# Performance work log

Hardware: AMD Instinct MI355X
Metric: run time of the kernel (lower is better)

The kernel has to match this reference:

```python
import jax, jax.numpy as jnp
import numpy as np
from jax import lax

B, C, H, W = 4, 256, 64, 64
C8 = C // 8  # 32


def setup_inputs() -> dict:
    key = jax.random.key(0)
    ks = jax.random.split(key, 8)
    x = jax.random.normal(ks[0], (B, C, H, W), jnp.float32)
    # 1x1 conv weights stored as [out_ch, in_ch]
    wb = jax.random.normal(ks[1], (C8, 2 * C), jnp.float32) * 0.02
    bb = jax.random.normal(ks[2], (C8,), jnp.float32) * 0.02
    wc = jax.random.normal(ks[3], (C8, 2 * C), jnp.float32) * 0.02
    bc = jax.random.normal(ks[4], (C8,), jnp.float32) * 0.02
    wd = jax.random.normal(ks[5], (C, 2 * C), jnp.float32) * 0.02
    bd = jax.random.normal(ks[6], (C,), jnp.float32) * 0.02
    alpha = jnp.float32(0.5)  # nn.Parameter(zeros(1)) at init; nonzero for a meaningful test
    return {"x": x, "wb": wb, "bb": bb, "wc": wc, "bc": bc, "wd": wd, "bd": bd, "alpha": alpha}


def reference(x, wb, bb, wc, bc, wd, bd, alpha):
    b, c, h, w = x.shape
    n = h * w
    pad = [(0, 0), (0, 0), (1, 1), (1, 1)]
    # F.avg_pool2d(k=3, s=1, p=1) with count_include_pad=True -> window-sum / 9
    x_avg = lax.reduce_window(x, 0.0, lax.add, (1, 1, 3, 3), (1, 1, 1, 1), pad) / 9.0
    x_max = lax.reduce_window(x, -jnp.inf, lax.max, (1, 1, 3, 3), (1, 1, 1, 1), pad)
    cat = jnp.concatenate([x_avg, x_max], axis=1)  # [B, 2C, H, W]
    catf = cat.reshape(b, 2 * c, n)                # [B, 2C, N]
    # 1x1 convs == per-pixel linear projections
    feat_b = jnp.einsum('oc,bcn->bon', wb, catf) + bb[None, :, None]  # [B, C8, N]
    feat_c = jnp.einsum('oc,bcn->bon', wc, catf) + bc[None, :, None]  # [B, C8, N]
    feat_d = jnp.einsum('oc,bcn->bon', wd, catf) + bd[None, :, None]  # [B, C,  N]
    # attention_s = softmax(feat_b^T @ feat_c) over last dim -> [B, N, N]
    attn = jax.nn.softmax(jnp.einsum('bon,bom->bnm', feat_b, feat_c), axis=-1)
    # feat_e = feat_d @ attn^T -> [B, C, N]
    feat_e = jnp.einsum('bcn,bmn->bcm', feat_d, attn).reshape(b, c, h, w)
    return alpha * feat_e + (1.0 - alpha) * x
```

## Files before the change

### kernel.cpp

```cpp
#include <hip/hip_runtime.h>
#include <hip/hip_bf16.h>

typedef __hip_bfloat16 bf16;
typedef __attribute__((ext_vector_type(8))) short s8v;
typedef __attribute__((ext_vector_type(4))) float f4v;

__device__ __forceinline__ ushort f2u(float f) {
    bf16 h = __float2bfloat16(f);
    return *(ushort*)&h;
}


__global__ __launch_bounds__(256) void pool_kernel(
    const float* __restrict__ x, ushort* __restrict__ cat,
    const float* __restrict__ wb, const float* __restrict__ wc,
    const float* __restrict__ wd, ushort* __restrict__ Wf) {
    int bid = blockIdx.x;
    int tid = threadIdx.x;
    if (bid >= 1024) {
        int f = (bid - 1024) * 4 + (tid >> 6);
        int l = tid & 63;
        int ot = f % 20, kc = f / 20;
        int o = ot * 16 + (l & 15);
        int k0 = kc * 32 + (l >> 4) * 8;
        const float* wr = (o < 32) ? wb + (size_t)o * 512
                        : (o < 64) ? wc + (size_t)(o - 32) * 512
                                   : wd + (size_t)(o - 64) * 512;
        float4 f0 = *(const float4*)(wr + k0);
        float4 f1 = *(const float4*)(wr + k0 + 4);
        ushort tmp[8] = {f2u(f0.x), f2u(f0.y), f2u(f0.z), f2u(f0.w),
                         f2u(f1.x), f2u(f1.y), f2u(f1.z), f2u(f1.w)};
        *(uint4*)(Wf + kc * 10240 + ot * 512 + l * 8) = *(uint4*)tmp;
        return;
    }
    __shared__ float Xs[3][64][66];
    int b = bid >> 8, h = (bid >> 2) & 63, cg = bid & 3;
    bool hasU = (h > 0), hasD = (h < 63);
    #pragma unroll
    for (int pp = 0; pp < 12; ++pp) {
        int linear = pp * 256 + tid;
        int w4 = linear & 15;
        int cs = (linear >> 4) & 63;
        int dh = linear >> 10;
        int hh = h + dh - 1;
        float4 f = {0.f, 0.f, 0.f, 0.f};
        if ((unsigned)hh < 64u)
            f = *(const float4*)(x + ((size_t)(b * 256 + cg * 64 + cs)) * 4096
                                 + hh * 64 + w4 * 4);
        Xs[dh][w4 * 4 + 0][cs] = f.x;
        Xs[dh][w4 * 4 + 1][cs] = f.y;
        Xs[dh][w4 * 4 + 2][cs] = f.z;
        Xs[dh][w4 * 4 + 3][cs] = f.w;
    }
    __syncthreads();
    int cs = tid & 63, ws = tid >> 6;
    float vs[18], vm[18];
    #pragma unroll
    for (int j = 0; j < 18; ++j) {
        int w = ws * 16 - 1 + j;
        if ((unsigned)w < 64u) {
            float u = Xs[0][w][cs], m = Xs[1][w][cs], d = Xs[2][w][cs];
            vs[j] = u + m + d;
            float mx = m;
            if (hasU) mx = fmaxf(mx, u);
            if (hasD) mx = fmaxf(mx, d);
            vm[j] = mx;
        } else { vs[j] = 0.f; vm[j] = -3.4e38f; }
    }
    size_t nb = ((size_t)b * 4096 + h * 64 + ws * 16) * 512 + cg * 64 + cs;
    #pragma unroll
    for (int i = 0; i < 16; ++i) {
        float sum = vs[i] + vs[i + 1] + vs[i + 2];
        float mx  = fmaxf(fmaxf(vm[i], vm[i + 1]), vm[i + 2]);
        cat[nb + (size_t)i * 512]       = f2u(sum * (1.f / 9.f));
        cat[nb + (size_t)i * 512 + 256] = f2u(mx);
    }
}

__global__ __launch_bounds__(256, 2) void proj_kernel(
    const ushort* __restrict__ cat, const ushort* __restrict__ Wf,
    const float* __restrict__ bb, const float* __restrict__ bc,
    const float* __restrict__ bd,
    ushort* __restrict__ Qb, ushort* __restrict__ Kb, ushort* __restrict__ Vf) {
    __shared__ __align__(16) ushort As[32][72];
    __shared__ __align__(16) ushort Vls[256][40];
    int tid = threadIdx.x;
    int l = tid & 63, w = tid >> 6;
    int lm = l & 15, q = l >> 4;
    int n0 = blockIdx.x * 32;
    f4v acc[2][5];
    #pragma unroll
    for (int mt = 0; mt < 2; ++mt)
        #pragma unroll
        for (int ot = 0; ot < 5; ++ot)
            #pragma unroll
            for (int i = 0; i < 4; ++i) acc[mt][ot][i] = 0.f;

    const ushort* wfb = Wf + (w * 5) * 512 + l * 8;
    int sr = tid >> 3, sko = (tid & 7) * 8;
    const ushort* srow = cat + (size_t)(n0 + sr) * 512 + sko;

    for (int kc = 0; kc < 8; ++kc) {
        *(uint4*)&As[sr][sko] = *(const uint4*)(srow + kc * 64);
        __syncthreads();
        #pragma unroll
        for (int ks = 0; ks < 2; ++ks) {
            int kci = kc * 2 + ks;
            s8v bf[5];
            #pragma unroll
            for (int ot = 0; ot < 5; ++ot)
                bf[ot] = *(const s8v*)(wfb + kci * 10240 + ot * 512);
            s8v a0 = *(const s8v*)&As[lm][ks * 32 + q * 8];
            s8v a1 = *(const s8v*)&As[16 + lm][ks * 32 + q * 8];
            #pragma unroll
            for (int ot = 0; ot < 5; ++ot) {
                acc[0][ot] = __builtin_amdgcn_mfma_f32_16x16x32_bf16(a0, bf[ot], acc[0][ot], 0, 0, 0);
                acc[1][ot] = __builtin_amdgcn_mfma_f32_16x16x32_bf16(a1, bf[ot], acc[1][ot], 0, 0, 0);
            }
        }
        __syncthreads();
    }
    #pragma unroll
    for (int ot = 0; ot < 5; ++ot) {
        int o = w * 80 + ot * 16 + lm;
        if (o < 32) {
            float bias = bb[o];
            #pragma unroll
            for (int mt = 0; mt < 2; ++mt)
                #pragma unroll
                for (int r = 0; r < 4; ++r)
                    Qb[(size_t)(n0 + mt * 16 + q * 4 + r) * 32 + o]
                        = f2u(acc[mt][ot][r] + bias);
        } else if (o < 64) {
            float bias = bc[o - 32];
            #pragma unroll
            for (int mt = 0; mt < 2; ++mt)
                #pragma unroll
                for (int r = 0; r < 4; ++r)
                    Kb[(size_t)(n0 + mt * 16 + q * 4 + r) * 32 + (o - 32)]
                        = f2u(acc[mt][ot][r] + bias);
        } else {
            int c = o - 64;
            float bias = bd[c];
            #pragma unroll
            for (int mt = 0; mt < 2; ++mt) {
                ushort tmp[4];
                #pragma unroll
                for (int r = 0; r < 4; ++r) tmp[r] = f2u(acc[mt][ot][r] + bias);
                *(uint2*)&Vls[c][mt * 16 + q * 4] = *(uint2*)tmp;
            }
        }
    }
    __syncthreads();
    {
        int bidx = n0 >> 12;
        size_t fb = ((size_t)bidx << 20) + (size_t)((n0 & 4095) >> 5) * 8192 + l * 8;
        #pragma unroll
        for (int i = 0; i < 4; ++i) {
            int cb = w * 4 + i;
            *(uint4*)(Vf + fb + cb * 512) = *(const uint4*)&Vls[cb * 16 + lm][q * 8];
        }
    }
}

__global__ __launch_bounds__(512, 2) void attn_kernel(
    const ushort* __restrict__ Qb, const ushort* __restrict__ Kb,
    const ushort* __restrict__ Vf, const float* __restrict__ x,
    const float* __restrict__ alphap, float* __restrict__ out) {
    __shared__ __align__(16) ushort Ps[2][64][72];
    __shared__ float Obuf[4][64][17];
    __shared__ float Lpart[4][64];
    __shared__ float Lrow[64];
    int tid = threadIdx.x;
    int l = tid & 63, w = tid >> 6;
    int lm = l & 15, q = l >> 4;
    int nsw = w & 3, kh = w >> 2;
    int bid = blockIdx.x;
    int xcd = bid & 7;
    int b = xcd & 3;
    int midx = (bid >> 3) + ((xcd >> 2) << 5);
    int m0 = midx << 6;
    size_t bN = (size_t)b << 12;

    s8v Qf[2];
    {
        const ushort* qb = Qb + (bN + m0 + kh * 32) * 32;
        Qf[0] = *(const s8v*)(qb + (size_t)(lm) * 32 + q * 8);
        Qf[1] = *(const s8v*)(qb + (size_t)(16 + lm) * 32 + q * 8);
    }
    const ushort* kbp = Kb + (bN + nsw * 16 + lm) * 32 + q * 8;
    const ushort* vfp = Vf + ((size_t)b << 20) + kh * 8192 + (nsw * 4) * 512 + l * 8;

    f4v acc[4][4];
    #pragma unroll
    for (int mt = 0; mt < 4; ++mt)
        #pragma unroll
        for (int ct = 0; ct < 4; ++ct)
            #pragma unroll
            for (int i = 0; i < 4; ++i) acc[mt][ct][i] = 0.f;
    float La0 = 0.f, La1 = 0.f;

    s8v kf0 = *(const s8v*)kbp;
    s8v kf1 = *(const s8v*)(kbp + 2048);
    s8v vfA[4], vfB[4];
    #pragma unroll
    for (int ct = 0; ct < 4; ++ct) vfA[ct] = *(const s8v*)(vfp + ct * 512);
    {
        f4v S0 = {0.f, 0.f, 0.f, 0.f}, S1 = {0.f, 0.f, 0.f, 0.f};
        S0 = __builtin_amdgcn_mfma_f32_16x16x32_bf16(kf0, Qf[0], S0, 0, 0, 0);
        S1 = __builtin_amdgcn_mfma_f32_16x16x32_bf16(kf0, Qf[1], S1, 0, 0, 0);
        ushort e0[4], e1[4];
        #pragma unroll
        for (int r = 0; r < 4; ++r) {
            float f0 = __expf(fminf(S0[r], 60.f));
            float f1 = __expf(fminf(S1[r], 60.f));
            La0 += f0; La1 += f1;
            e0[r] = f2u(f0); e1[r] = f2u(f1);
        }
        *(uint2*)&Ps[0][kh * 32 + lm][nsw * 16 + q * 4]      = *(uint2*)e0;
        *(uint2*)&Ps[0][kh * 32 + 16 + lm][nsw * 16 + q * 4] = *(uint2*)e1;
    }
    __syncthreads();

#define TILE_BODY(TT, KFS, KFP, VCUR, VNXT)                                       \
    {                                                                             \
        int p = (TT) & 1;                                                         \
        if ((TT) < 63) {                                                          \
            f4v S0 = {0.f, 0.f, 0.f, 0.f}, S1 = {0.f, 0.f, 0.f, 0.f};             \
            S0 = __builtin_amdgcn_mfma_f32_16x16x32_bf16(KFS, Qf[0], S0, 0, 0, 0);\
            S1 = __builtin_amdgcn_mfma_f32_16x16x32_bf16(KFS, Qf[1], S1, 0, 0, 0);\
            ushort e0[4], e1[4];                                                  \
            _Pragma("unroll")                                                     \
            for (int r = 0; r < 4; ++r) {                                         \
                float f0 = __expf(fminf(S0[r], 60.f));                            \
                float f1 = __expf(fminf(S1[r], 60.f));                            \
                La0 += f0; La1 += f1;                                             \
                e0[r] = f2u(f0); e1[r] = f2u(f1);                                 \
            }                                                                     \
            *(uint2*)&Ps[1 - p][kh * 32 + lm][nsw * 16 + q * 4]      = *(uint2*)e0;\
            *(uint2*)&Ps[1 - p][kh * 32 + 16 + lm][nsw * 16 + q * 4] = *(uint2*)e1;\
        }                                                                         \
        if ((TT) < 62) KFP = *(const s8v*)(kbp + (size_t)((TT) + 2) * 2048);      \
        if ((TT) < 63) {                                                          \
            const ushort* vn = vfp + (size_t)((TT) + 1) * 16384;                  \
            _Pragma("unroll")                                                     \
            for (int ct = 0; ct < 4; ++ct)                                        \
                VNXT[ct] = *(const s8v*)(vn + ct * 512);                          \
        }                                                                         \
        s8v Af0 = *(const s8v*)&Ps[p][lm][kh * 32 + q * 8];                       \
        s8v Af1 = *(const s8v*)&Ps[p][16 + lm][kh * 32 + q * 8];                  \
        s8v Af2 = *(const s8v*)&Ps[p][32 + lm][kh * 32 + q * 8];                  \
        s8v Af3 = *(const s8v*)&Ps[p][48 + lm][kh * 32 + q * 8];                  \
        _Pragma("unroll")                                                         \
        for (int ct = 0; ct < 4; ++ct) {                                          \
            acc[0][ct] = __builtin_amdgcn_mfma_f32_16x16x32_bf16(Af0, VCUR[ct], acc[0][ct], 0, 0, 0); \
            acc[1][ct] = __builtin_amdgcn_mfma_f32_16x16x32_bf16(Af1, VCUR[ct], acc[1][ct], 0, 0, 0); \
            acc[2][ct] = __builtin_amdgcn_mfma_f32_16x16x32_bf16(Af2, VCUR[ct], acc[2][ct], 0, 0, 0); \
            acc[3][ct] = __builtin_amdgcn_mfma_f32_16x16x32_bf16(Af3, VCUR[ct], acc[3][ct], 0, 0, 0); \
        }                                                                         \
        __syncthreads();                                                          \
    }

    for (int t = 0; t < 64; t += 2) {
        TILE_BODY(t,     kf1, kf0, vfA, vfB);
        TILE_BODY(t + 1, kf0, kf1, vfB, vfA);
    }
#undef TILE_BODY

    La0 += __shfl_xor(La0, 16, 64); La0 += __shfl_xor(La0, 32, 64);
    La1 += __shfl_xor(La1, 16, 64); La1 += __shfl_xor(La1, 32, 64);
    if (q == 0) {
        Lpart[nsw][kh * 32 + lm]      = La0;
        Lpart[nsw][kh * 32 + 16 + lm] = La1;
    }
    __syncthreads();
    if (tid < 64)
        Lrow[tid] = Lpart[0][tid] + Lpart[1][tid] + Lpart[2][tid] + Lpart[3][tid];
    __syncthreads();
    #pragma unroll
    for (int ct = 0; ct < 4; ++ct) {
        if (kh == 1) {
            #pragma unroll
            for (int mt = 0; mt < 4; ++mt)
                #pragma unroll
                for (int r = 0; r < 4; ++r)
                    Obuf[nsw][mt * 16 + q * 4 + r][lm] = acc[mt][ct][r];
        }
        __syncthreads();
        if (kh == 0) {
            #pragma unroll
            for (int mt = 0; mt < 4; ++mt)
                #pragma unroll
                for (int r = 0; r < 4; ++r)
                    acc[mt][ct][r] += Obuf[nsw][mt * 16 + q * 4 + r][lm];
        }
        __syncthreads();
    }
    if (kh == 0) {
        float alpha = alphap[0];
        float ra = 1.f - alpha;
        #pragma unroll
        for (int mt = 0; mt < 4; ++mt) {
            float L0 = Lrow[mt * 16 + q * 4 + 0];
            float L1 = Lrow[mt * 16 + q * 4 + 1];
            float L2 = Lrow[mt * 16 + q * 4 + 2];
            float L3 = Lrow[mt * 16 + q * 4 + 3];
            #pragma unroll
            for (int ct = 0; ct < 4; ++ct) {
                int cc = nsw * 64 + ct * 16 + lm;
                size_t base = ((size_t)(b * 256 + cc)) * 4096 + m0 + mt * 16 + q * 4;
                float4 xv = *(const float4*)(x + base);
                float4 ov;
                ov.x = alpha * (acc[mt][ct][0] / L0) + ra * xv.x;
                ov.y = alpha * (acc[mt][ct][1] / L1) + ra * xv.y;
                ov.z = alpha * (acc[mt][ct][2] / L2) + ra * xv.z;
                ov.w = alpha * (acc[mt][ct][3] / L3) + ra * xv.w;
                *(float4*)(out + base) = ov;
            }
        }
    }
}

extern "C" void kernel_launch(void* const* d_in, const int* in_sizes, int n_in,
                              void* d_out, int out_size, void* d_ws, size_t ws_size,
                              hipStream_t stream) {
    const float* x  = (const float*)d_in[0];
    const float* wb = (const float*)d_in[1];
    const float* bb = (const float*)d_in[2];
    const float* wc = (const float*)d_in[3];
    const float* bc = (const float*)d_in[4];
    const float* wd = (const float*)d_in[5];
    const float* bd = (const float*)d_in[6];
    const float* al = (const float*)d_in[7];
    float* out = (float*)d_out;

    char* ws = (char*)d_ws;
    ushort* cat = (ushort*)ws;
    ushort* Qb  = (ushort*)(ws + 16777216);
    ushort* Kb  = (ushort*)(ws + 17825792);
    ushort* Vf  = (ushort*)(ws + 18874368);
    ushort* Wf  = (ushort*)(ws + 27262976);

    pool_kernel<<<dim3(1104), dim3(256), 0, stream>>>(x, cat, wb, wc, wd, Wf);
    proj_kernel<<<dim3(512), dim3(256), 0, stream>>>(cat, Wf, bb, bc, bd,
                                                     Qb, Kb, Vf);
    attn_kernel<<<dim3(256), dim3(512), 0, stream>>>(Qb, Kb, Vf, x, al, out);
}
```

Measured before the change: 164.6 us.

## Double attention block to 1024 threads, split S and channels across more waves

The attention kernel now runs 16 waves per block instead of 8. Each wave computes one 16x16 S tile instead of two and accumulates 32 output channels instead of 64, which halves per-wave MFMA work and register pressure. The exp/P-store for the next tile is moved after the PV MFMAs so it can overlap with them, and the final normalisation uses reciprocals instead of divisions. The cost is more block-wide synchronisation across twice as many waves, plus a larger Obuf in shared memory. The launch bound of (1024,4) may force a register cap that causes spills.

```diff
diff --git a/kernel.cpp b/kernel.cpp
--- a/kernel.cpp
+++ b/kernel.cpp
@@ -163,18 +163,19 @@
     }
 }
 
-__global__ __launch_bounds__(512, 2) void attn_kernel(
+__global__ __launch_bounds__(1024, 4) void attn_kernel(
     const ushort* __restrict__ Qb, const ushort* __restrict__ Kb,
     const ushort* __restrict__ Vf, const float* __restrict__ x,
     const float* __restrict__ alphap, float* __restrict__ out) {
     __shared__ __align__(16) ushort Ps[2][64][72];
-    __shared__ float Obuf[4][64][17];
+    __shared__ float Obuf[8][64][17];
     __shared__ float Lpart[4][64];
     __shared__ float Lrow[64];
     int tid = threadIdx.x;
     int l = tid & 63, w = tid >> 6;
     int lm = l & 15, q = l >> 4;
-    int nsw = w & 3, kh = w >> 2;
+    int nsw = w & 3, msw = w >> 2;
+    int cs = w & 7, kh = w >> 3;
     int bid = blockIdx.x;
     int xcd = bid & 7;
     int b = xcd & 3;
@@ -182,82 +183,69 @@
     int m0 = midx << 6;
     size_t bN = (size_t)b << 12;
 
-    s8v Qf[2];
-    {
-        const ushort* qb = Qb + (bN + m0 + kh * 32) * 32;
-        Qf[0] = *(const s8v*)(qb + (size_t)(lm) * 32 + q * 8);
-        Qf[1] = *(const s8v*)(qb + (size_t)(16 + lm) * 32 + q * 8);
-    }
+    s8v Qf = *(const s8v*)(Qb + (bN + m0 + msw * 16 + lm) * 32 + q * 8);
     const ushort* kbp = Kb + (bN + nsw * 16 + lm) * 32 + q * 8;
-    const ushort* vfp = Vf + ((size_t)b << 20) + kh * 8192 + (nsw * 4) * 512 + l * 8;
-
-    f4v acc[4][4];
+    const ushort* vfp = Vf + ((size_t)b << 20) + kh * 8192 + (2 * cs) * 512 + l * 8;
+
+    f4v acc[4][2];
     #pragma unroll
     for (int mt = 0; mt < 4; ++mt)
         #pragma unroll
-        for (int ct = 0; ct < 4; ++ct)
+        for (int ct = 0; ct < 2; ++ct)
             #pragma unroll
             for (int i = 0; i < 4; ++i) acc[mt][ct][i] = 0.f;
-    float La0 = 0.f, La1 = 0.f;
+    float La = 0.f;
 
     s8v kf0 = *(const s8v*)kbp;
     s8v kf1 = *(const s8v*)(kbp + 2048);
-    s8v vfA[4], vfB[4];
-    #pragma unroll
-    for (int ct = 0; ct < 4; ++ct) vfA[ct] = *(const s8v*)(vfp + ct * 512);
+    s8v vfA[2], vfB[2];
+    vfA[0] = *(const s8v*)(vfp);
+    vfA[1] = *(const s8v*)(vfp + 512);
     {
-        f4v S0 = {0.f, 0.f, 0.f, 0.f}, S1 = {0.f, 0.f, 0.f, 0.f};
-        S0 = __builtin_amdgcn_mfma_f32_16x16x32_bf16(kf0, Qf[0], S0, 0, 0, 0);
-        S1 = __builtin_amdgcn_mfma_f32_16x16x32_bf16(kf0, Qf[1], S1, 0, 0, 0);
-        ushort e0[4], e1[4];
+        f4v S = {0.f, 0.f, 0.f, 0.f};
+        S = __builtin_amdgcn_mfma_f32_16x16x32_bf16(kf0, Qf, S, 0, 0, 0);
+        ushort e0[4];
         #pragma unroll
         for (int r = 0; r < 4; ++r) {
-            float f0 = __expf(fminf(S0[r], 60.f));
-            float f1 = __expf(fminf(S1[r], 60.f));
-            La0 += f0; La1 += f1;
-            e0[r] = f2u(f0); e1[r] = f2u(f1);
-        }
-        *(uint2*)&Ps[0][kh * 32 + lm][nsw * 16 + q * 4]      = *(uint2*)e0;
-        *(uint2*)&Ps[0][kh * 32 + 16 + lm][nsw * 16 + q * 4] = *(uint2*)e1;
+            float f0 = __expf(fminf(S[r], 60.f));
+            La += f0; e0[r] = f2u(f0);
+        }
+        *(uint2*)&Ps[0][msw * 16 + lm][nsw * 16 + q * 4] = *(uint2*)e0;
     }
     __syncthreads();
 
 #define TILE_BODY(TT, KFS, KFP, VCUR, VNXT)                                       \
     {                                                                             \
         int p = (TT) & 1;                                                         \
-        if ((TT) < 63) {                                                          \
-            f4v S0 = {0.f, 0.f, 0.f, 0.f}, S1 = {0.f, 0.f, 0.f, 0.f};             \
-            S0 = __builtin_amdgcn_mfma_f32_16x16x32_bf16(KFS, Qf[0], S0, 0, 0, 0);\
-            S1 = __builtin_amdgcn_mfma_f32_16x16x32_bf16(KFS, Qf[1], S1, 0, 0, 0);\
-            ushort e0[4], e1[4];                                                  \
-            _Pragma("unroll")                                                     \
-            for (int r = 0; r < 4; ++r) {                                         \
-                float f0 = __expf(fminf(S0[r], 60.f));                            \
-                float f1 = __expf(fminf(S1[r], 60.f));                            \
-                La0 += f0; La1 += f1;                                             \
-                e0[r] = f2u(f0); e1[r] = f2u(f1);                                 \
-            }                                                                     \
-            *(uint2*)&Ps[1 - p][kh * 32 + lm][nsw * 16 + q * 4]      = *(uint2*)e0;\
-            *(uint2*)&Ps[1 - p][kh * 32 + 16 + lm][nsw * 16 + q * 4] = *(uint2*)e1;\
-        }                                                                         \
+        f4v S = {0.f, 0.f, 0.f, 0.f};                                             \
+        if ((TT) < 63)                                                            \
+            S = __builtin_amdgcn_mfma_f32_16x16x32_bf16(KFS, Qf, S, 0, 0, 0);     \
         if ((TT) < 62) KFP = *(const s8v*)(kbp + (size_t)((TT) + 2) * 2048);      \
         if ((TT) < 63) {                                                          \
             const ushort* vn = vfp + (size_t)((TT) + 1) * 16384;                  \
-            _Pragma("unroll")                                                     \
-            for (int ct = 0; ct < 4; ++ct)                                        \
-                VNXT[ct] = *(const s8v*)(vn + ct * 512);                          \
+            VNXT[0] = *(const s8v*)(vn);                                          \
+            VNXT[1] = *(const s8v*)(vn + 512);                                    \
         }                                                                         \
         s8v Af0 = *(const s8v*)&Ps[p][lm][kh * 32 + q * 8];                       \
         s8v Af1 = *(const s8v*)&Ps[p][16 + lm][kh * 32 + q * 8];                  \
         s8v Af2 = *(const s8v*)&Ps[p][32 + lm][kh * 32 + q * 8];                  \
         s8v Af3 = *(const s8v*)&Ps[p][48 + lm][kh * 32 + q * 8];                  \
         _Pragma("unroll")                                                         \
-        for (int ct = 0; ct < 4; ++ct) {                                          \
+        for (int ct = 0; ct < 2; ++ct) {                                          \
             acc[0][ct] = __builtin_amdgcn_mfma_f32_16x16x32_bf16(Af0, VCUR[ct], acc[0][ct], 0, 0, 0); \
             acc[1][ct] = __builtin_amdgcn_mfma_f32_16x16x32_bf16(Af1, VCUR[ct], acc[1][ct], 0, 0, 0); \
             acc[2][ct] = __builtin_amdgcn_mfma_f32_16x16x32_bf16(Af2, VCUR[ct], acc[2][ct], 0, 0, 0); \
             acc[3][ct] = __builtin_amdgcn_mfma_f32_16x16x32_bf16(Af3, VCUR[ct], acc[3][ct], 0, 0, 0); \
         }                                                                         \
+        if ((TT) < 63) {                                                          \
+            ushort e0[4];                                                         \
+            _Pragma("unroll")                                                     \
+            for (int r = 0; r < 4; ++r) {                                         \
+                float f0 = __expf(fminf(S[r], 60.f));                             \
+                La += f0; e0[r] = f2u(f0);                                        \
+            }                                                                     \
+            *(uint2*)&Ps[1 - p][msw * 16 + lm][nsw * 16 + q * 4] = *(uint2*)e0;   \
+        }                                                                         \
         __syncthreads();                                                          \
     }
 
@@ -267,24 +255,21 @@
     }
 #undef TILE_BODY
 
-    La0 += __shfl_xor(La0, 16, 64); La0 += __shfl_xor(La0, 32, 64);
-    La1 += __shfl_xor(La1, 16, 64); La1 += __shfl_xor(La1, 32, 64);
-    if (q == 0) {
-        Lpart[nsw][kh * 32 + lm]      = La0;
-        Lpart[nsw][kh * 32 + 16 + lm] = La1;
-    }
+    La += __shfl_xor(La, 16, 64);
+    La += __shfl_xor(La, 32, 64);
+    if (q == 0) Lpart[nsw][msw * 16 + lm] = La;
     __syncthreads();
     if (tid < 64)
         Lrow[tid] = Lpart[0][tid] + Lpart[1][tid] + Lpart[2][tid] + Lpart[3][tid];
     __syncthreads();
     #pragma unroll
-    for (int ct = 0; ct < 4; ++ct) {
+    for (int ct = 0; ct < 2; ++ct) {
         if (kh == 1) {
             #pragma unroll
             for (int mt = 0; mt < 4; ++mt)
                 #pragma unroll
                 for (int r = 0; r < 4; ++r)
-                    Obuf[nsw][mt * 16 + q * 4 + r][lm] = acc[mt][ct][r];
+                    Obuf[cs][mt * 16 + q * 4 + r][lm] = acc[mt][ct][r];
         }
         __syncthreads();
         if (kh == 0) {
@@ -292,7 +277,7 @@
             for (int mt = 0; mt < 4; ++mt)
                 #pragma unroll
                 for (int r = 0; r < 4; ++r)
-                    acc[mt][ct][r] += Obuf[nsw][mt * 16 + q * 4 + r][lm];
+                    acc[mt][ct][r] += Obuf[cs][mt * 16 + q * 4 + r][lm];
         }
         __syncthreads();
     }
@@ -301,20 +286,20 @@
         float ra = 1.f - alpha;
         #pragma unroll
         for (int mt = 0; mt < 4; ++mt) {
-            float L0 = Lrow[mt * 16 + q * 4 + 0];
-            float L1 = Lrow[mt * 16 + q * 4 + 1];
-            float L2 = Lrow[mt * 16 + q * 4 + 2];
-            float L3 = Lrow[mt * 16 + q * 4 + 3];
-            #pragma unroll
-            for (int ct = 0; ct < 4; ++ct) {
-                int cc = nsw * 64 + ct * 16 + lm;
+            float i0 = 1.f / Lrow[mt * 16 + q * 4 + 0];
+            float i1 = 1.f / Lrow[mt * 16 + q * 4 + 1];
+            float i2 = 1.f / Lrow[mt * 16 + q * 4 + 2];
+            float i3 = 1.f / Lrow[mt * 16 + q * 4 + 3];
+            #pragma unroll
+            for (int ct = 0; ct < 2; ++ct) {
+                int cc = cs * 32 + ct * 16 + lm;
                 size_t base = ((size_t)(b * 256 + cc)) * 4096 + m0 + mt * 16 + q * 4;
                 float4 xv = *(const float4*)(x + base);
                 float4 ov;
-                ov.x = alpha * (acc[mt][ct][0] / L0) + ra * xv.x;
-                ov.y = alpha * (acc[mt][ct][1] / L1) + ra * xv.y;
-                ov.z = alpha * (acc[mt][ct][2] / L2) + ra * xv.z;
-                ov.w = alpha * (acc[mt][ct][3] / L3) + ra * xv.w;
+                ov.x = alpha * (acc[mt][ct][0] * i0) + ra * xv.x;
+                ov.y = alpha * (acc[mt][ct][1] * i1) + ra * xv.y;
+                ov.z = alpha * (acc[mt][ct][2] * i2) + ra * xv.z;
+                ov.w = alpha * (acc[mt][ct][3] * i3) + ra * xv.w;
                 *(float4*)(out + base) = ov;
             }
         }
@@ -344,5 +329,5 @@
     pool_kernel<<<dim3(1104), dim3(256), 0, stream>>>(x, cat, wb, wc, wd, Wf);
     proj_kernel<<<dim3(512), dim3(256), 0, stream>>>(cat, Wf, bb, bc, bd,
                                                      Qb, Kb, Vf);
-    attn_kernel<<<dim3(256), dim3(512), 0, stream>>>(Qb, Kb, Vf, x, al, out);
-}
+    attn_kernel<<<dim3(256), dim3(1024), 0, stream>>>(Qb, Kb, Vf, x, al, out);
+}
```

Result: slower. 173.4 us (+5.3%).

## Triple-buffer attention P tiles and interleave score and PV MFMA phases

Applied to the files above, without the earlier changes.

Moves the attention main loop from a double-buffered P tile to a three-slot rotating buffer, so score computation runs two tiles ahead of the PV accumulation. Within each tile, half of the waves issue the PV MFMA cluster before the exp/softmax tail and the other half after it, with s_setprio raised around the MFMA cluster, so matrix and vector work from different waves can overlap. K and V prefetch now goes two tiles ahead, and the barrier becomes a hand-written lgkmcnt wait plus s_barrier. The cost is more LDS, more registers held for prefetched operands, and harder-to-read control flow.

```diff
diff --git a/kernel.cpp b/kernel.cpp
--- a/kernel.cpp
+++ b/kernel.cpp
@@ -167,7 +167,7 @@
     const ushort* __restrict__ Qb, const ushort* __restrict__ Kb,
     const ushort* __restrict__ Vf, const float* __restrict__ x,
     const float* __restrict__ alphap, float* __restrict__ out) {
-    __shared__ __align__(16) ushort Ps[2][64][72];
+    __shared__ __align__(16) ushort Ps[3][64][72];
     __shared__ float Obuf[4][64][17];
     __shared__ float Lpart[4][64];
     __shared__ float Lrow[64];
@@ -200,72 +200,115 @@
             for (int i = 0; i < 4; ++i) acc[mt][ct][i] = 0.f;
     float La0 = 0.f, La1 = 0.f;
 
-    s8v kf0 = *(const s8v*)kbp;
-    s8v kf1 = *(const s8v*)(kbp + 2048);
+    ushort* pA = &Ps[0][0][0];
+    ushort* pB = &Ps[1][0][0];
+    ushort* pC = &Ps[2][0][0];
+
+#define SCORE_TAIL(S0, S1, PDST)                                                  \
+    {                                                                             \
+        ushort e0[4], e1[4];                                                      \
+        _Pragma("unroll")                                                         \
+        for (int r = 0; r < 4; ++r) {                                             \
+            float f0 = __expf(fminf(S0[r], 60.f));                                \
+            float f1 = __expf(fminf(S1[r], 60.f));                                \
+            La0 += f0; La1 += f1;                                                 \
+            e0[r] = f2u(f0); e1[r] = f2u(f1);                                     \
+        }                                                                         \
+        *(uint2*)(PDST + (kh * 32 + lm) * 72 + nsw * 16 + q * 4)      = *(uint2*)e0; \
+        *(uint2*)(PDST + (kh * 32 + 16 + lm) * 72 + nsw * 16 + q * 4) = *(uint2*)e1; \
+    }
+
+    s8v k0 = *(const s8v*)kbp;
+    s8v k1 = *(const s8v*)(kbp + 2048);
+    s8v kfA = *(const s8v*)(kbp + 2 * 2048);
+    s8v kfB = *(const s8v*)(kbp + 3 * 2048);
     s8v vfA[4], vfB[4];
     #pragma unroll
     for (int ct = 0; ct < 4; ++ct) vfA[ct] = *(const s8v*)(vfp + ct * 512);
+    #pragma unroll
+    for (int ct = 0; ct < 4; ++ct) vfB[ct] = *(const s8v*)(vfp + 16384 + ct * 512);
     {
         f4v S0 = {0.f, 0.f, 0.f, 0.f}, S1 = {0.f, 0.f, 0.f, 0.f};
-        S0 = __builtin_amdgcn_mfma_f32_16x16x32_bf16(kf0, Qf[0], S0, 0, 0, 0);
-        S1 = __builtin_amdgcn_mfma_f32_16x16x32_bf16(kf0, Qf[1], S1, 0, 0, 0);
-        ushort e0[4], e1[4];
-        #pragma unroll
-        for (int r = 0; r < 4; ++r) {
-            float f0 = __expf(fminf(S0[r], 60.f));
-            float f1 = __expf(fminf(S1[r], 60.f));
-            La0 += f0; La1 += f1;
-            e0[r] = f2u(f0); e1[r] = f2u(f1);
-        }
-        *(uint2*)&Ps[0][kh * 32 + lm][nsw * 16 + q * 4]      = *(uint2*)e0;
-        *(uint2*)&Ps[0][kh * 32 + 16 + lm][nsw * 16 + q * 4] = *(uint2*)e1;
-    }
-    __syncthreads();
-
-#define TILE_BODY(TT, KFS, KFP, VCUR, VNXT)                                       \
+        S0 = __builtin_amdgcn_mfma_f32_16x16x32_bf16(k0, Qf[0], S0, 0, 0, 0);
+        S1 = __builtin_amdgcn_mfma_f32_16x16x32_bf16(k0, Qf[1], S1, 0, 0, 0);
+        SCORE_TAIL(S0, S1, pA);
+    }
+    {
+        f4v S0 = {0.f, 0.f, 0.f, 0.f}, S1 = {0.f, 0.f, 0.f, 0.f};
+        S0 = __builtin_amdgcn_mfma_f32_16x16x32_bf16(k1, Qf[0], S0, 0, 0, 0);
+        S1 = __builtin_amdgcn_mfma_f32_16x16x32_bf16(k1, Qf[1], S1, 0, 0, 0);
+        SCORE_TAIL(S0, S1, pB);
+    }
+    __syncthreads();
+
+    const ushort* kpa = kbp + 4 * 2048;
+    const ushort* kpb = kbp + 5 * 2048;
+    const ushort* vpa = vfp + 2 * 16384;
+    const ushort* vpb = vfp + 3 * 16384;
+
+#define PV_CLUSTER(VCUR)                                                          \
+    __builtin_amdgcn_s_setprio(1);                                                \
+    _Pragma("unroll")                                                             \
+    for (int ct = 0; ct < 4; ++ct) {                                              \
+        acc[0][ct] = __builtin_amdgcn_mfma_f32_16x16x32_bf16(Af0, VCUR[ct], acc[0][ct], 0, 0, 0); \
+        acc[1][ct] = __builtin_amdgcn_mfma_f32_16x16x32_bf16(Af1, VCUR[ct], acc[1][ct], 0, 0, 0); \
+        acc[2][ct] = __builtin_amdgcn_mfma_f32_16x16x32_bf16(Af2, VCUR[ct], acc[2][ct], 0, 0, 0); \
+        acc[3][ct] = __builtin_amdgcn_mfma_f32_16x16x32_bf16(Af3, VCUR[ct], acc[3][ct], 0, 0, 0); \
+    }                                                                             \
+    __builtin_amdgcn_s_setprio(0);
+
+#define TILE_BODY(TT, KFS, VCUR, KREF, VREF)                                      \
     {                                                                             \
-        int p = (TT) & 1;                                                         \
-        if ((TT) < 63) {                                                          \
+        if (kh == 0) {                                                            \
+            s8v Af0 = *(const s8v*)(pA + (lm) * 72 + q * 8);                      \
+            s8v Af1 = *(const s8v*)(pA + (16 + lm) * 72 + q * 8);                 \
+            s8v Af2 = *(const s8v*)(pA + (32 + lm) * 72 + q * 8);                 \
+            s8v Af3 = *(const s8v*)(pA + (48 + lm) * 72 + q * 8);                 \
             f4v S0 = {0.f, 0.f, 0.f, 0.f}, S1 = {0.f, 0.f, 0.f, 0.f};             \
-            S0 = __builtin_amdgcn_mfma_f32_16x16x32_bf16(KFS, Qf[0], S0, 0, 0, 0);\
-            S1 = __builtin_amdgcn_mfma_f32_16x16x32_bf16(KFS, Qf[1], S1, 0, 0, 0);\
-            ushort e0[4], e1[4];                                                  \
-            _Pragma("unroll")                                                     \
-            for (int r = 0; r < 4; ++r) {                                         \
-                float f0 = __expf(fminf(S0[r], 60.f));                            \
-                float f1 = __expf(fminf(S1[r], 60.f));                            \
-                La0 += f0; La1 += f1;                                             \
-                e0[r] = f2u(f0); e1[r] = f2u(f1);                                 \
+            if ((TT) < 62) {                                                      \
+                S0 = __builtin_amdgcn_mfma_f32_16x16x32_bf16(KFS, Qf[0], S0, 0, 0, 0); \
+                S1 = __builtin_amdgcn_mfma_f32_16x16x32_bf16(KFS, Qf[1], S1, 0, 0, 0); \
             }                                                                     \
-            *(uint2*)&Ps[1 - p][kh * 32 + lm][nsw * 16 + q * 4]      = *(uint2*)e0;\
-            *(uint2*)&Ps[1 - p][kh * 32 + 16 + lm][nsw * 16 + q * 4] = *(uint2*)e1;\
+            PV_CLUSTER(VCUR)                                                      \
+            if ((TT) < 62) SCORE_TAIL(S0, S1, pC)                                 \
+            if ((TT) < 60) { KFS = *(const s8v*)(KREF); KREF += 4096; }           \
+            if ((TT) < 62) {                                                      \
+                _Pragma("unroll")                                                 \
+                for (int ct = 0; ct < 4; ++ct)                                    \
+                    VCUR[ct] = *(const s8v*)(VREF + ct * 512);                    \
+                VREF += 32768;                                                    \
+            }                                                                     \
+        } else {                                                                  \
+            f4v S0 = {0.f, 0.f, 0.f, 0.f}, S1 = {0.f, 0.f, 0.f, 0.f};             \
+            if ((TT) < 62) {                                                      \
+                S0 = __builtin_amdgcn_mfma_f32_16x16x32_bf16(KFS, Qf[0], S0, 0, 0, 0); \
+                S1 = __builtin_amdgcn_mfma_f32_16x16x32_bf16(KFS, Qf[1], S1, 0, 0, 0); \
+                SCORE_TAIL(S0, S1, pC)                                            \
+            }                                                                     \
+            s8v Af0 = *(const s8v*)(pA + (lm) * 72 + 32 + q * 8);                 \
+            s8v Af1 = *(const s8v*)(pA + (16 + lm) * 72 + 32 + q * 8);            \
+            s8v Af2 = *(const s8v*)(pA + (32 + lm) * 72 + 32 + q * 8);            \
+            s8v Af3 = *(const s8v*)(pA + (48 + lm) * 72 + 32 + q * 8);            \
+            PV_CLUSTER(VCUR)                                                      \
+            if ((TT) < 60) { KFS = *(const s8v*)(KREF); KREF += 4096; }           \
+            if ((TT) < 62) {                                                      \
+                _Pragma("unroll")                                                 \
+                for (int ct = 0; ct < 4; ++ct)                                    \
+                    VCUR[ct] = *(const s8v*)(VREF + ct * 512);                    \
+                VREF += 32768;                                                    \
+            }                                                                     \
         }                                                                         \
-        if ((TT) < 62) KFP = *(const s8v*)(kbp + (size_t)((TT) + 2) * 2048);      \
-        if ((TT) < 63) {                                                          \
-            const ushort* vn = vfp + (size_t)((TT) + 1) * 16384;                  \
-            _Pragma("unroll")                                                     \
-            for (int ct = 0; ct < 4; ++ct)                                        \
-                VNXT[ct] = *(const s8v*)(vn + ct * 512);                          \
-        }                                                                         \
-        s8v Af0 = *(const s8v*)&Ps[p][lm][kh * 32 + q * 8];                       \
-        s8v Af1 = *(const s8v*)&Ps[p][16 + lm][kh * 32 + q * 8];                  \
-        s8v Af2 = *(const s8v*)&Ps[p][32 + lm][kh * 32 + q * 8];                  \
-        s8v Af3 = *(const s8v*)&Ps[p][48 + lm][kh * 32 + q * 8];                  \
-        _Pragma("unroll")                                                         \
-        for (int ct = 0; ct < 4; ++ct) {                                          \
-            acc[0][ct] = __builtin_amdgcn_mfma_f32_16x16x32_bf16(Af0, VCUR[ct], acc[0][ct], 0, 0, 0); \
-            acc[1][ct] = __builtin_amdgcn_mfma_f32_16x16x32_bf16(Af1, VCUR[ct], acc[1][ct], 0, 0, 0); \
-            acc[2][ct] = __builtin_amdgcn_mfma_f32_16x16x32_bf16(Af2, VCUR[ct], acc[2][ct], 0, 0, 0); \
-            acc[3][ct] = __builtin_amdgcn_mfma_f32_16x16x32_bf16(Af3, VCUR[ct], acc[3][ct], 0, 0, 0); \
-        }                                                                         \
-        __syncthreads();                                                          \
+        asm volatile("s_waitcnt lgkmcnt(0)\n\ts_barrier" ::: "memory");           \
+        { ushort* rot_ = pA; pA = pB; pB = pC; pC = rot_; }                       \
     }
 
     for (int t = 0; t < 64; t += 2) {
-        TILE_BODY(t,     kf1, kf0, vfA, vfB);
-        TILE_BODY(t + 1, kf0, kf1, vfB, vfA);
+        TILE_BODY(t,     kfA, vfA, kpa, vpa);
+        TILE_BODY(t + 1, kfB, vfB, kpb, vpb);
     }
 #undef TILE_BODY
+#undef PV_CLUSTER
+#undef SCORE_TAIL
 
     La0 += __shfl_xor(La0, 16, 64); La0 += __shfl_xor(La0, 32, 64);
     La1 += __shfl_xor(La1, 16, 64); La1 += __shfl_xor(La1, 32, 64);
```

Measured after the change: 165.0 us. Within noise of the previous version (+0.2%).
